# Optimization experiments

Measured on AMD Instinct MI355X. Metric: run time of the kernel, lower is better.

## Reference

```python
import jax, jax.numpy as jnp
import numpy as np
from jax import lax

N, L, V, ES, HS = 16384, 512, 32000, 32, 64


def setup_inputs() -> dict:
    key = jax.random.key(0)
    k_tok, k_len, k_emb, k_wih, k_whh, k_bih, k_bhh = jax.random.split(key, 7)
    # valid tokens in [1, V) so that (x != 0).sum(1) == true prefix length
    tok = jax.random.randint(k_tok, (N, L), 1, V)
    lengths = jax.random.randint(k_len, (N,), 0, L + 1)  # includes empty seqs
    x = jnp.where(jnp.arange(L)[None, :] < lengths[:, None], tok, 0)
    s = 0.1
    embedding = jax.random.normal(k_emb, (V, ES), dtype=jnp.float32) * s
    w_ih = jax.random.normal(k_wih, (3 * HS, ES), dtype=jnp.float32) * s  # [r|z|n] stacked (torch order)
    w_hh = jax.random.normal(k_whh, (3 * HS, HS), dtype=jnp.float32) * s
    b_ih = jax.random.normal(k_bih, (3 * HS,), dtype=jnp.float32) * s
    b_hh = jax.random.normal(k_bhh, (3 * HS,), dtype=jnp.float32) * s
    return {"x": x, "embedding": embedding, "w_ih": w_ih, "w_hh": w_hh,
            "b_ih": b_ih, "b_hh": b_hh}


def reference(x, embedding, w_ih, w_hh, b_ih, b_hh):
    # Faithful math: final GRU hidden state over the nonzero prefix of each row;
    # rows with length 0 return zeros (h0). Equivalent to bucketed
    # pack_padded_sequence + GRU + scatter of final hidden states.
    n, l = x.shape
    hs = w_hh.shape[1]
    lengths = (x != 0).sum(axis=1)  # [n]

    def step(h, inp):
        t, xt = inp                      # xt: [n] token ids at time t
        e = embedding[xt]                # [n, es] gather
        gx = e @ w_ih.T + b_ih           # [n, 3*hs]
        gh = h @ w_hh.T + b_hh           # [n, 3*hs]
        xr, xz, xn = jnp.split(gx, 3, axis=-1)
        hr, hz, hn = jnp.split(gh, 3, axis=-1)
        r = jax.nn.sigmoid(xr + hr)
        z = jax.nn.sigmoid(xz + hz)
        ng = jnp.tanh(xn + r * hn)
        h_new = (1.0 - z) * ng + z * h   # torch GRU update
        h = jnp.where((t < lengths)[:, None], h_new, h)  # freeze past length
        return h, None

    h0 = jnp.zeros((n, hs), dtype=embedding.dtype)
    hT, _ = lax.scan(step, h0, (jnp.arange(l), x.T))
    return hT
```

## Files before the change

kernel.cpp:

```cpp
#include <hip/hip_runtime.h>

#define N_SEQ 16384
#define LSEQ  512
#define VOCAB 32000
#define ES    32
#define HS    64
#define LDH   72

#define SC_RZ (-1.4426950408889634f)
#define SC_N  (-2.8853900817779268f)

typedef _Float16 v8h __attribute__((ext_vector_type(8)));
typedef float    v4f __attribute__((ext_vector_type(4)));

#define NLB (N_SEQ / 4)
#define NEB (VOCAB * ES / 256)
__global__ __launch_bounds__(256) void k_prep(const int* __restrict__ x,
                                              const float* __restrict__ emb,
                                              const float* __restrict__ whh,
                                              const float* __restrict__ wih,
                                              int* __restrict__ len,
                                              int* __restrict__ hist,
                                              _Float16* __restrict__ ef,
                                              _Float16* __restrict__ wpk,
                                              _Float16* __restrict__ wpe){
  int b = blockIdx.x;
  if (b < NLB){
    int wid  = (b * 256 + threadIdx.x) >> 6;
    int lane = threadIdx.x & 63;
    const int* xr = x + (size_t)wid * LSEQ;
    int cnt = 0;
    #pragma unroll
    for (int j = 0; j < 8; ++j) cnt += (xr[lane + 64*j] != 0) ? 1 : 0;
    #pragma unroll
    for (int o = 32; o; o >>= 1) cnt += __shfl_down(cnt, o, 64);
    if (lane == 0){ len[wid] = cnt; atomicAdd(&hist[cnt], 1); }
  } else if (b < NLB + NEB){
    int i = (b - NLB) * 256 + threadIdx.x;
    ef[i] = (_Float16)emb[i];
  } else if (b < NLB + NEB + 6){
    int tid = (b - NLB - NEB) * 256 + threadIdx.x;
    int f = tid >> 6, l = tid & 63;
    int jt = f >> 1, kf = f & 1;
    float sc = (jt < 8) ? SC_RZ : SC_N;
    #pragma unroll
    for (int i = 0; i < 8; ++i){
      int row = jt * 16 + (l & 15);
      int col = kf * 32 + (l >> 4) * 8 + i;
      wpk[(size_t)tid * 8 + i] = (_Float16)(sc * whh[row * HS + col]);
    }
  } else {
    int tid = (b - NLB - NEB - 6) * 256 + threadIdx.x;
    int tile = tid >> 6, l = tid & 63;
    float sc = ((tile >> 2) < 2) ? SC_RZ : SC_N;
    #pragma unroll
    for (int i = 0; i < 8; ++i){
      int row = tile * 16 + (l & 15);
      int col = (l >> 4) * 8 + i;
      wpe[(size_t)tid * 8 + i] = (_Float16)(sc * wih[row * ES + col]);
    }
  }
}

__global__ __launch_bounds__(1024) void k_scan(const int* __restrict__ hist,
                                               int* __restrict__ offs){
  __shared__ int buf[1024];
  int i = threadIdx.x;
  buf[i] = (i < 513) ? hist[i] : 0;
  __syncthreads();
  for (int d = 1; d < 1024; d <<= 1){
    int v = (i >= d) ? buf[i - d] : 0;
    __syncthreads();
    buf[i] += v;
    __syncthreads();
  }
  if (i < 513) offs[i] = (i == 0) ? 0 : buf[i - 1];
}

__global__ __launch_bounds__(256) void k_scatter(const int* __restrict__ len,
                                                 int* __restrict__ offs,
                                                 int* __restrict__ perm){
  int i = blockIdx.x * 256 + threadIdx.x;
  int l = len[i];
  int pos = atomicAdd(&offs[l], 1);
  perm[pos] = i;
}

__global__ __launch_bounds__(256, 4) void k_gru(
    const int* __restrict__ x, const _Float16* __restrict__ ef,
    const _Float16* __restrict__ wpk, const _Float16* __restrict__ wpe,
    const float* __restrict__ bih, const float* __restrict__ bhh,
    const int* __restrict__ perm, const int* __restrict__ len,
    float* __restrict__ out)
{
  __shared__ __align__(16) _Float16 hb[2][16 * LDH];
  int qt   = threadIdx.x >> 6;
  int w = blockIdx.x >> 8, cq = blockIdx.x & 255;
  int rank = w * 256 + ((w & 1) ? (255 - cq) : cq);
  int grp  = 1023 - rank;
  int lane = threadIdx.x & 63;
  int q = lane >> 4, c = lane & 15;
  int uu = qt*16 + c;

  v8h bfh[3][2], bfe[3];
  #pragma unroll
  for (int g = 0; g < 3; ++g){
    int tile = g*4 + qt;
    #pragma unroll
    for (int kf = 0; kf < 2; ++kf)
      bfh[g][kf] = *(const v8h*)(wpk + ((size_t)(tile*2 + kf)*64 + lane)*8);
    bfe[g] = *(const v8h*)(wpe + ((size_t)tile*64 + lane)*8);
  }

  int sq[4], ln[4];
  #pragma unroll
  for (int r = 0; r < 4; ++r){
    int s = perm[grp * 16 + q*4 + r];
    sq[r] = s;
    ln[r] = len[s];
  }
  float br  = SC_RZ * (bih[uu]      + bhh[uu]);
  float bz  = SC_RZ * (bih[HS + uu] + bhh[HS + uu]);
  float ben = SC_N  *  bih[2*HS + uu];
  float bhn = SC_N  *  bhh[2*HS + uu];
  v4f brq  = {br, br, br, br};
  v4f bzq  = {bz, bz, bz, bz};
  v4f benq = {ben, ben, ben, ben};
  v4f bhnq = {bhn, bhn, bhn, bhn};

  float h[4];
  #pragma unroll
  for (int r = 0; r < 4; ++r) h[r] = 0.f;

  for (int i = threadIdx.x; i < 16*LDH; i += 256) hb[0][i] = (_Float16)0.f;
  __syncthreads();

  int tmax = max(max(ln[0], ln[1]), max(ln[2], ln[3]));
  tmax = max(tmax, __shfl_xor(tmax, 16, 64));
  tmax = max(tmax, __shfl_xor(tmax, 32, 64));
  int tmin = min(min(ln[0], ln[1]), min(ln[2], ln[3]));
  tmin = min(tmin, __shfl_xor(tmin, 16, 64));
  tmin = min(tmin, __shfl_xor(tmin, 32, 64));

  const int* xr = x + (size_t)perm[grp * 16 + c] * LSEQ;

  v8h aec, aen;
  int tk1, tk2;
  v4f pra, prb, pza, pzb, dea, deb;
  {
    int tk0 = xr[0];
    aec = *(const v8h*)(ef + (size_t)tk0 * ES + q*8);
    tk1 = xr[1];
    pra = __builtin_amdgcn_mfma_f32_16x16x32_f16(aec, bfe[0], brq,  0,0,0);
    pza = __builtin_amdgcn_mfma_f32_16x16x32_f16(aec, bfe[1], bzq,  0,0,0);
    dea = __builtin_amdgcn_mfma_f32_16x16x32_f16(aec, bfe[2], benq, 0,0,0);
  }

  #define GRU_STEP(FREEZE, AEN, PRR, PRZ, DEN, PRRn, PRZn, DENn, TKN_, TKNN_, RB, WB) \
  {                                                                            \
    AEN = *(const v8h*)(ef + (size_t)TKN_ * ES + q*8);       \
    int t2 = min(t + 2, LSEQ - 1);                                             \
    TKNN_ = xr[t2];                                             \
    v8h a0 = *(const v8h*)(&hb[RB][c*LDH + q*8]);                              \
    v8h a1 = *(const v8h*)(&hb[RB][c*LDH + 32 + q*8]);                         \
    v4f zr  = __builtin_amdgcn_mfma_f32_16x16x32_f16(a1, bfh[0][1], PRR, 0,0,0);\
    v4f Dr  = __builtin_amdgcn_mfma_f32_16x16x32_f16(a0, bfh[0][0], zr,  0,0,0);\
    v4f zz  = __builtin_amdgcn_mfma_f32_16x16x32_f16(a1, bfh[1][1], PRZ, 0,0,0);\
    v4f Dz  = __builtin_amdgcn_mfma_f32_16x16x32_f16(a0, bfh[1][0], zz,  0,0,0);\
    v4f zh  = __builtin_amdgcn_mfma_f32_16x16x32_f16(a1, bfh[2][1], bhnq,0,0,0);\
    v4f Dhn = __builtin_amdgcn_mfma_f32_16x16x32_f16(a0, bfh[2][0], zh,  0,0,0);\
    _Pragma("unroll")                                                          \
    for (int r = 0; r < 4; ++r){                                               \
      float rg   = __builtin_amdgcn_rcpf(1.f + __builtin_amdgcn_exp2f(Dr[r])); \
      float zg   = __builtin_amdgcn_rcpf(1.f + __builtin_amdgcn_exp2f(Dz[r])); \
      float te   = __builtin_amdgcn_exp2f(DEN[r] + rg * Dhn[r]);               \
      float ng   = (1.f - te) * __builtin_amdgcn_rcpf(1.f + te);               \
      float hnew = ng + zg * (h[r] - ng);                                      \
      h[r]       = (FREEZE && t >= ln[r]) ? h[r] : hnew;                       \
    }                                                                          \
    PRRn = __builtin_amdgcn_mfma_f32_16x16x32_f16(AEN, bfe[0], brq,  0,0,0);   \
    PRZn = __builtin_amdgcn_mfma_f32_16x16x32_f16(AEN, bfe[1], bzq,  0,0,0);   \
    DENn = __builtin_amdgcn_mfma_f32_16x16x32_f16(AEN, bfe[2], benq, 0,0,0);   \
    _Pragma("unroll")                                                          \
    for (int r = 0; r < 4; ++r)                                                \
      hb[WB][(q*4 + r)*LDH + uu] = (_Float16)h[r];                             \
    __syncthreads();                                                           \
  }

  int t = 0;
  for (; t + 1 < tmin; ){
    GRU_STEP(0, aen, pra, pza, dea, prb, pzb, deb, tk1, tk2, 0, 1); ++t;
    GRU_STEP(0, aec, prb, pzb, deb, pra, pza, dea, tk2, tk1, 1, 0); ++t;
  }
  for (; t + 1 < tmax; ){
    GRU_STEP(1, aen, pra, pza, dea, prb, pzb, deb, tk1, tk2, 0, 1); ++t;
    GRU_STEP(1, aec, prb, pzb, deb, pra, pza, dea, tk2, tk1, 1, 0); ++t;
  }
  if (t < tmax){
    GRU_STEP(1, aen, pra, pza, dea, prb, pzb, deb, tk1, tk2, 0, 1); ++t;
  }
  #undef GRU_STEP

  #pragma unroll
  for (int r = 0; r < 4; ++r)
    out[(size_t)sq[r] * HS + uu] = h[r];
}

extern "C" void kernel_launch(void* const* d_in, const int* in_sizes, int n_in,
                              void* d_out, int out_size, void* d_ws, size_t ws_size,
                              hipStream_t stream){
  const int*   x   = (const int*)  d_in[0];
  const float* emb = (const float*)d_in[1];
  const float* wih = (const float*)d_in[2];
  const float* whh = (const float*)d_in[3];
  const float* bih = (const float*)d_in[4];
  const float* bhh = (const float*)d_in[5];
  float* out = (float*)d_out;

  char* ws = (char*)d_ws;
  size_t off = 0;
  _Float16* ef  = (_Float16*)(ws + off);  off += (size_t)VOCAB * ES * sizeof(_Float16);
  _Float16* wpk = (_Float16*)(ws + off);  off += (size_t)24 * 64 * 8 * sizeof(_Float16);
  _Float16* wpe = (_Float16*)(ws + off);  off += (size_t)12 * 64 * 8 * sizeof(_Float16);
  off = (off + 255) & ~(size_t)255;
  int* len  = (int*)(ws + off);           off += (size_t)N_SEQ * sizeof(int);
  int* perm = (int*)(ws + off);           off += (size_t)N_SEQ * sizeof(int);
  int* hist = (int*)(ws + off);           off += 513 * sizeof(int);
  off = (off + 255) & ~(size_t)255;
  int* offs = (int*)(ws + off);           off += 513 * sizeof(int);

  hipMemsetAsync(hist, 0, 513 * sizeof(int), stream);
  k_prep   <<<NLB + NEB + 9, 256, 0, stream>>>(x, emb, whh, wih, len, hist, ef, wpk, wpe);
  k_scan   <<<1,            1024, 0, stream>>>(hist, offs);
  k_scatter<<<N_SEQ / 256,   256, 0, stream>>>(len, offs, perm);
  k_gru    <<<N_SEQ / 16,    256, 0, stream>>>(x, ef, wpk, wpe, bih, bhh, perm, len, out);
}
```

Before: 324.8 us.

## Process two independent 16-sequence groups per block to interleave recurrent chains

Each block now advances two groups of 16 sorted sequences in lockstep, issuing both groups' MFMA chains and gate math together so the independent work hides MFMA and transcendental latency within one wave. Grid size is halved, launch bounds drop to 2 blocks per CU, and the per-step __syncthreads is replaced by an inline lgkmcnt wait plus s_barrier. The input projection is now recomputed at the start of each step instead of being prefetched a step ahead, and tanh uses a 2/(1+e)-1 form. Trade-offs are higher register pressure, fewer resident blocks, and per-block step counts set by the longest of 32 sequences instead of 16.

```diff
diff --git a/kernel.cpp b/kernel.cpp
--- a/kernel.cpp
+++ b/kernel.cpp
@@ -86,18 +86,19 @@
   perm[pos] = i;
 }
 
-__global__ __launch_bounds__(256, 4) void k_gru(
+__global__ __launch_bounds__(256, 2) void k_gru(
     const int* __restrict__ x, const _Float16* __restrict__ ef,
     const _Float16* __restrict__ wpk, const _Float16* __restrict__ wpe,
     const float* __restrict__ bih, const float* __restrict__ bhh,
     const int* __restrict__ perm, const int* __restrict__ len,
     float* __restrict__ out)
 {
-  __shared__ __align__(16) _Float16 hb[2][16 * LDH];
+  __shared__ __align__(16) _Float16 hb[2][2][16 * LDH];
   int qt   = threadIdx.x >> 6;
   int w = blockIdx.x >> 8, cq = blockIdx.x & 255;
   int rank = w * 256 + ((w & 1) ? (255 - cq) : cq);
-  int grp  = 1023 - rank;
+  int pr   = 511 - rank;
+  int gA = pr * 2, gB = pr * 2 + 1;
   int lane = threadIdx.x & 63;
   int q = lane >> 4, c = lane & 15;
   int uu = qt*16 + c;
@@ -112,12 +113,11 @@
     bfe[g] = *(const v8h*)(wpe + ((size_t)tile*64 + lane)*8);
   }
 
-  int sq[4], ln[4];
+  int sqA[4], lnA[4], sqB[4], lnB[4];
   #pragma unroll
   for (int r = 0; r < 4; ++r){
-    int s = perm[grp * 16 + q*4 + r];
-    sq[r] = s;
-    ln[r] = len[s];
+    int sA = perm[gA * 16 + q*4 + r];  sqA[r] = sA;  lnA[r] = len[sA];
+    int sB = perm[gB * 16 + q*4 + r];  sqB[r] = sB;  lnB[r] = len[sB];
   }
   float br  = SC_RZ * (bih[uu]      + bhh[uu]);
   float bz  = SC_RZ * (bih[HS + uu] + bhh[HS + uu]);
@@ -128,82 +128,109 @@
   v4f benq = {ben, ben, ben, ben};
   v4f bhnq = {bhn, bhn, bhn, bhn};
 
-  float h[4];
-  #pragma unroll
-  for (int r = 0; r < 4; ++r) h[r] = 0.f;
-
-  for (int i = threadIdx.x; i < 16*LDH; i += 256) hb[0][i] = (_Float16)0.f;
+  float hA[4], hB[4];
+  #pragma unroll
+  for (int r = 0; r < 4; ++r){ hA[r] = 0.f; hB[r] = 0.f; }
+
+  for (int i = threadIdx.x; i < 16*LDH; i += 256){
+    hb[0][0][i] = (_Float16)0.f;
+    hb[1][0][i] = (_Float16)0.f;
+  }
   __syncthreads();
 
-  int tmax = max(max(ln[0], ln[1]), max(ln[2], ln[3]));
+  int tmax = max(max(lnA[0], lnA[1]), max(lnA[2], lnA[3]));
+  tmax = max(tmax, max(max(lnB[0], lnB[1]), max(lnB[2], lnB[3])));
   tmax = max(tmax, __shfl_xor(tmax, 16, 64));
   tmax = max(tmax, __shfl_xor(tmax, 32, 64));
-  int tmin = min(min(ln[0], ln[1]), min(ln[2], ln[3]));
+  int tmin = min(min(lnA[0], lnA[1]), min(lnA[2], lnA[3]));
+  tmin = min(tmin, min(min(lnB[0], lnB[1]), min(lnB[2], lnB[3])));
   tmin = min(tmin, __shfl_xor(tmin, 16, 64));
   tmin = min(tmin, __shfl_xor(tmin, 32, 64));
 
-  const int* xr = x + (size_t)perm[grp * 16 + c] * LSEQ;
-
-  v8h aec, aen;
-  int tk1, tk2;
-  v4f pra, prb, pza, pzb, dea, deb;
+  const int* xrA = x + (size_t)perm[gA * 16 + c] * LSEQ;
+  const int* xrB = x + (size_t)perm[gB * 16 + c] * LSEQ;
+
+  v8h aecA, aenA, aecB, aenB;
+  int tkA1, tkA2, tkB1, tkB2;
   {
-    int tk0 = xr[0];
-    aec = *(const v8h*)(ef + (size_t)tk0 * ES + q*8);
-    tk1 = xr[1];
-    pra = __builtin_amdgcn_mfma_f32_16x16x32_f16(aec, bfe[0], brq,  0,0,0);
-    pza = __builtin_amdgcn_mfma_f32_16x16x32_f16(aec, bfe[1], bzq,  0,0,0);
-    dea = __builtin_amdgcn_mfma_f32_16x16x32_f16(aec, bfe[2], benq, 0,0,0);
-  }
-
-  #define GRU_STEP(FREEZE, AEN, PRR, PRZ, DEN, PRRn, PRZn, DENn, TKN_, TKNN_, RB, WB) \
+    aecA = *(const v8h*)(ef + (size_t)xrA[0] * ES + q*8);
+    aecB = *(const v8h*)(ef + (size_t)xrB[0] * ES + q*8);
+    tkA1 = xrA[1];  tkB1 = xrB[1];
+  }
+
+  #define LDS_BARRIER() __asm__ volatile("s_waitcnt lgkmcnt(0)\n\ts_barrier" ::: "memory")
+
+  #define DUAL_STEP(FREEZE, AECA, AENA, TKA1_, TKA2_, AECB, AENB, TKB1_, TKB2_, RB, WB) \
   {                                                                            \
-    AEN = *(const v8h*)(ef + (size_t)TKN_ * ES + q*8);       \
+    AENA = *(const v8h*)(ef + (size_t)TKA1_ * ES + q*8);                       \
+    AENB = *(const v8h*)(ef + (size_t)TKB1_ * ES + q*8);                       \
     int t2 = min(t + 2, LSEQ - 1);                                             \
-    TKNN_ = xr[t2];                                             \
-    v8h a0 = *(const v8h*)(&hb[RB][c*LDH + q*8]);                              \
-    v8h a1 = *(const v8h*)(&hb[RB][c*LDH + 32 + q*8]);                         \
-    v4f zr  = __builtin_amdgcn_mfma_f32_16x16x32_f16(a1, bfh[0][1], PRR, 0,0,0);\
-    v4f Dr  = __builtin_amdgcn_mfma_f32_16x16x32_f16(a0, bfh[0][0], zr,  0,0,0);\
-    v4f zz  = __builtin_amdgcn_mfma_f32_16x16x32_f16(a1, bfh[1][1], PRZ, 0,0,0);\
-    v4f Dz  = __builtin_amdgcn_mfma_f32_16x16x32_f16(a0, bfh[1][0], zz,  0,0,0);\
-    v4f zh  = __builtin_amdgcn_mfma_f32_16x16x32_f16(a1, bfh[2][1], bhnq,0,0,0);\
-    v4f Dhn = __builtin_amdgcn_mfma_f32_16x16x32_f16(a0, bfh[2][0], zh,  0,0,0);\
+    TKA2_ = xrA[t2];  TKB2_ = xrB[t2];                                         \
+    v4f prA = __builtin_amdgcn_mfma_f32_16x16x32_f16(AECA, bfe[0], brq,  0,0,0);\
+    v4f pzA = __builtin_amdgcn_mfma_f32_16x16x32_f16(AECA, bfe[1], bzq,  0,0,0);\
+    v4f deA = __builtin_amdgcn_mfma_f32_16x16x32_f16(AECA, bfe[2], benq, 0,0,0);\
+    v4f prB = __builtin_amdgcn_mfma_f32_16x16x32_f16(AECB, bfe[0], brq,  0,0,0);\
+    v4f pzB = __builtin_amdgcn_mfma_f32_16x16x32_f16(AECB, bfe[1], bzq,  0,0,0);\
+    v4f deB = __builtin_amdgcn_mfma_f32_16x16x32_f16(AECB, bfe[2], benq, 0,0,0);\
+    v8h a0A = *(const v8h*)(&hb[0][RB][c*LDH + q*8]);                          \
+    v8h a1A = *(const v8h*)(&hb[0][RB][c*LDH + 32 + q*8]);                     \
+    v8h a0B = *(const v8h*)(&hb[1][RB][c*LDH + q*8]);                          \
+    v8h a1B = *(const v8h*)(&hb[1][RB][c*LDH + 32 + q*8]);                     \
+    v4f zrA  = __builtin_amdgcn_mfma_f32_16x16x32_f16(a1A, bfh[0][1], prA, 0,0,0);\
+    v4f DrA  = __builtin_amdgcn_mfma_f32_16x16x32_f16(a0A, bfh[0][0], zrA, 0,0,0);\
+    v4f zzA  = __builtin_amdgcn_mfma_f32_16x16x32_f16(a1A, bfh[1][1], pzA, 0,0,0);\
+    v4f DzA  = __builtin_amdgcn_mfma_f32_16x16x32_f16(a0A, bfh[1][0], zzA, 0,0,0);\
+    v4f zhA  = __builtin_amdgcn_mfma_f32_16x16x32_f16(a1A, bfh[2][1], bhnq,0,0,0);\
+    v4f DhnA = __builtin_amdgcn_mfma_f32_16x16x32_f16(a0A, bfh[2][0], zhA, 0,0,0);\
+    v4f zrB  = __builtin_amdgcn_mfma_f32_16x16x32_f16(a1B, bfh[0][1], prB, 0,0,0);\
+    v4f DrB  = __builtin_amdgcn_mfma_f32_16x16x32_f16(a0B, bfh[0][0], zrB, 0,0,0);\
+    v4f zzB  = __builtin_amdgcn_mfma_f32_16x16x32_f16(a1B, bfh[1][1], pzB, 0,0,0);\
+    v4f DzB  = __builtin_amdgcn_mfma_f32_16x16x32_f16(a0B, bfh[1][0], zzB, 0,0,0);\
+    v4f zhB  = __builtin_amdgcn_mfma_f32_16x16x32_f16(a1B, bfh[2][1], bhnq,0,0,0);\
+    v4f DhnB = __builtin_amdgcn_mfma_f32_16x16x32_f16(a0B, bfh[2][0], zhB, 0,0,0);\
     _Pragma("unroll")                                                          \
     for (int r = 0; r < 4; ++r){                                               \
-      float rg   = __builtin_amdgcn_rcpf(1.f + __builtin_amdgcn_exp2f(Dr[r])); \
-      float zg   = __builtin_amdgcn_rcpf(1.f + __builtin_amdgcn_exp2f(Dz[r])); \
-      float te   = __builtin_amdgcn_exp2f(DEN[r] + rg * Dhn[r]);               \
-      float ng   = (1.f - te) * __builtin_amdgcn_rcpf(1.f + te);               \
-      float hnew = ng + zg * (h[r] - ng);                                      \
-      h[r]       = (FREEZE && t >= ln[r]) ? h[r] : hnew;                       \
+      float rgA = __builtin_amdgcn_rcpf(1.f + __builtin_amdgcn_exp2f(DrA[r])); \
+      float zgA = __builtin_amdgcn_rcpf(1.f + __builtin_amdgcn_exp2f(DzA[r])); \
+      float teA = __builtin_amdgcn_exp2f(deA[r] + rgA * DhnA[r]);              \
+      float ngA = fmaf(2.f, __builtin_amdgcn_rcpf(1.f + teA), -1.f);           \
+      float hnA = ngA + zgA * (hA[r] - ngA);                                   \
+      hA[r] = (FREEZE && t >= lnA[r]) ? hA[r] : hnA;                           \
+      float rgB = __builtin_amdgcn_rcpf(1.f + __builtin_amdgcn_exp2f(DrB[r])); \
+      float zgB = __builtin_amdgcn_rcpf(1.f + __builtin_amdgcn_exp2f(DzB[r])); \
+      float teB = __builtin_amdgcn_exp2f(deB[r] + rgB * DhnB[r]);              \
+      float ngB = fmaf(2.f, __builtin_amdgcn_rcpf(1.f + teB), -1.f);           \
+      float hnB = ngB + zgB * (hB[r] - ngB);                                   \
+      hB[r] = (FREEZE && t >= lnB[r]) ? hB[r] : hnB;                           \
     }                                                                          \
-    PRRn = __builtin_amdgcn_mfma_f32_16x16x32_f16(AEN, bfe[0], brq,  0,0,0);   \
-    PRZn = __builtin_amdgcn_mfma_f32_16x16x32_f16(AEN, bfe[1], bzq,  0,0,0);   \
-    DENn = __builtin_amdgcn_mfma_f32_16x16x32_f16(AEN, bfe[2], benq, 0,0,0);   \
     _Pragma("unroll")                                                          \
-    for (int r = 0; r < 4; ++r)                                                \
-      hb[WB][(q*4 + r)*LDH + uu] = (_Float16)h[r];                             \
-    __syncthreads();                                                           \
+    for (int r = 0; r < 4; ++r){                                               \
+      hb[0][WB][(q*4 + r)*LDH + uu] = (_Float16)hA[r];                         \
+      hb[1][WB][(q*4 + r)*LDH + uu] = (_Float16)hB[r];                         \
+    }                                                                          \
+    LDS_BARRIER();                                                             \
   }
 
   int t = 0;
   for (; t + 1 < tmin; ){
-    GRU_STEP(0, aen, pra, pza, dea, prb, pzb, deb, tk1, tk2, 0, 1); ++t;
-    GRU_STEP(0, aec, prb, pzb, deb, pra, pza, dea, tk2, tk1, 1, 0); ++t;
+    DUAL_STEP(0, aecA, aenA, tkA1, tkA2, aecB, aenB, tkB1, tkB2, 0, 1); ++t;
+    DUAL_STEP(0, aenA, aecA, tkA2, tkA1, aenB, aecB, tkB2, tkB1, 1, 0); ++t;
   }
   for (; t + 1 < tmax; ){
-    GRU_STEP(1, aen, pra, pza, dea, prb, pzb, deb, tk1, tk2, 0, 1); ++t;
-    GRU_STEP(1, aec, prb, pzb, deb, pra, pza, dea, tk2, tk1, 1, 0); ++t;
+    DUAL_STEP(1, aecA, aenA, tkA1, tkA2, aecB, aenB, tkB1, tkB2, 0, 1); ++t;
+    DUAL_STEP(1, aenA, aecA, tkA2, tkA1, aenB, aecB, tkB2, tkB1, 1, 0); ++t;
   }
   if (t < tmax){
-    GRU_STEP(1, aen, pra, pza, dea, prb, pzb, deb, tk1, tk2, 0, 1); ++t;
-  }
-  #undef GRU_STEP
-
-  #pragma unroll
-  for (int r = 0; r < 4; ++r)
-    out[(size_t)sq[r] * HS + uu] = h[r];
+    DUAL_STEP(1, aecA, aenA, tkA1, tkA2, aecB, aenB, tkB1, tkB2, 0, 1); ++t;
+  }
+  #undef DUAL_STEP
+  #undef LDS_BARRIER
+
+  #pragma unroll
+  for (int r = 0; r < 4; ++r){
+    out[(size_t)sqA[r] * HS + uu] = hA[r];
+    out[(size_t)sqB[r] * HS + uu] = hB[r];
+  }
 }
 
 extern "C" void kernel_launch(void* const* d_in, const int* in_sizes, int n_in,
@@ -233,5 +260,5 @@
   k_prep   <<<NLB + NEB + 9, 256, 0, stream>>>(x, emb, whh, wih, len, hist, ef, wpk, wpe);
   k_scan   <<<1,            1024, 0, stream>>>(hist, offs);
   k_scatter<<<N_SEQ / 256,   256, 0, stream>>>(len, offs, perm);
-  k_gru    <<<N_SEQ / 16,    256, 0, stream>>>(x, ef, wpk, wpe, bih, bhh, perm, len, out);
-}
+  k_gru    <<<N_SEQ / 32,    256, 0, stream>>>(x, ef, wpk, wpe, bih, bhh, perm, len, out);
+}
```

After: 386.0 us. +18.9%, slower.
